# Optimization experiments

Measured on AMD Instinct MI355X. Metric: run time of the kernel, lower is better.

## Reference

```python
import jax, jax.numpy as jnp
import numpy as np

NUM_PAGES = 1024
PAGE_SIZE = 64
KV_HEADS = 8
HEAD_DIM = 128
NUM_TOKENS = 8192


def setup_inputs() -> dict:
    key = jax.random.key(0)
    k1, k2, k3 = jax.random.split(key, 3)
    kv_pages = jnp.zeros((NUM_PAGES, PAGE_SIZE, 2 * KV_HEADS, HEAD_DIM), dtype=jnp.float32)
    new_k = jax.random.normal(k1, (NUM_TOKENS, KV_HEADS, HEAD_DIM), dtype=jnp.float32)
    new_v = jax.random.normal(k2, (NUM_TOKENS, KV_HEADS, HEAD_DIM), dtype=jnp.float32)
    # distinct random destination slots (irregular but deterministic scatter);
    # mark a small tail as padding (-1) to exercise the drop path.
    dests = jax.random.permutation(k3, NUM_PAGES * PAGE_SIZE)[:NUM_TOKENS].astype(jnp.int32)
    pad = jnp.arange(NUM_TOKENS) >= (NUM_TOKENS - 128)
    token_dests = jnp.where(pad, jnp.int32(-1), dests)
    return {"kv_pages": kv_pages, "new_k": new_k, "new_v": new_v, "token_dests": token_dests}


def reference(kv_pages, new_k, new_v, token_dests):
    # kv_pages: [num_pages, page_size, 2*kv_heads, head_dim]
    # new_k/new_v: [tok, kv_heads, head_dim]; token_dests: i32[tok] flat slot index (-1 = pad)
    num_pages, page_size = kv_pages.shape[0], kv_pages.shape[1]
    kv_heads = new_k.shape[1]
    valid = token_dests >= 0
    t_pages = jnp.where(valid, token_dests // page_size, num_pages)   # OOB -> dropped
    t_slots = jnp.where(valid, token_dests % page_size, page_size)
    out = kv_pages.at[t_pages, t_slots, :kv_heads].set(new_k, mode="drop")
    out = out.at[t_pages, t_slots, kv_heads:].set(new_v, mode="drop")
    return out
```

## Files before the change

kernel.cpp:

```cpp
#include <hip/hip_runtime.h>


__global__ void kv_scatter_kernel(const float4* __restrict__ new_k,
                                  const float4* __restrict__ new_v,
                                  const int* __restrict__ dests,
                                  float4* __restrict__ out,
                                  int num_slots) {
    const int t = blockIdx.x;
    const int d = dests[t];
    if (d < 0 || d >= num_slots) return;

    const float4* __restrict__ k = new_k + (size_t)t * 256;
    const float4* __restrict__ v = new_v + (size_t)t * 256;
    float4* __restrict__ o = out + (size_t)d * 512;

    const int i = threadIdx.x;
    o[i]       = k[i];
    o[i + 256] = v[i];
}

extern "C" void kernel_launch(void* const* d_in, const int* in_sizes, int n_in,
                              void* d_out, int out_size, void* d_ws, size_t ws_size,
                              hipStream_t stream) {
    const float* kv_pages = (const float*)d_in[0];
    const float* new_k    = (const float*)d_in[1];
    const float* new_v    = (const float*)d_in[2];
    const int*   dests    = (const int*)d_in[3];

    const int num_tokens = in_sizes[3];
    const int row_floats = 2 * 8 * 128;
    const int num_slots  = out_size / row_floats;

    hipMemcpyAsync(d_out, kv_pages, (size_t)out_size * sizeof(float),
                   hipMemcpyDeviceToDevice, stream);

    kv_scatter_kernel<<<num_tokens, 256, 0, stream>>>(
        (const float4*)new_k, (const float4*)new_v, dests,
        (float4*)d_out, num_slots);
}
```

Before: 234.0 us.

## Fuse page copy and scatter via inverse slot map with nontemporal accesses

Builds an inverse map from destination slot to token in workspace, then a single grid-stride kernel writes every output row once, reading either the new K/V row or the original page row. This avoids copying the full cache and then overwriting the scattered slots, so the scattered rows are written once instead of twice. Loads and stores use nontemporal builtins to limit cache pollution. It adds two small kernel launches and depends on enough workspace being available, falling back to the old path otherwise.

```diff
diff --git a/kernel.cpp b/kernel.cpp
--- a/kernel.cpp
+++ b/kernel.cpp
@@ -1,19 +1,56 @@
 #include <hip/hip_runtime.h>
 
 
-__global__ void kv_scatter_kernel(const float4* __restrict__ new_k,
-                                  const float4* __restrict__ new_v,
+typedef float f4 __attribute__((ext_vector_type(4)));
+
+__global__ void inv_init_kernel(int* __restrict__ inv, int num_slots) {
+    const int stride = gridDim.x * blockDim.x;
+    for (int s = blockIdx.x * blockDim.x + threadIdx.x; s < num_slots; s += stride)
+        inv[s] = -1;
+}
+
+__global__ void inv_scatter_kernel(const int* __restrict__ dests, int num_tokens,
+                                   int* __restrict__ inv, int num_slots) {
+    const int t = blockIdx.x * blockDim.x + threadIdx.x;
+    if (t >= num_tokens) return;
+    const int d = dests[t];
+    if (d >= 0 && d < num_slots) inv[d] = t;
+}
+
+__global__ void fused_copy_scatter(const f4* __restrict__ kv_pages,
+                                   const f4* __restrict__ new_k,
+                                   const f4* __restrict__ new_v,
+                                   const int* __restrict__ inv,
+                                   f4* __restrict__ out,
+                                   int num_slots) {
+    const int i = threadIdx.x;
+    for (int slot = blockIdx.x; slot < num_slots; slot += gridDim.x) {
+        const int t = inv[slot];
+        f4* o = out + (size_t)slot * 512;
+        if (t >= 0) {
+            const f4* k = new_k + (size_t)t * 256;
+            const f4* v = new_v + (size_t)t * 256;
+            __builtin_nontemporal_store(__builtin_nontemporal_load(k + i), o + i);
+            __builtin_nontemporal_store(__builtin_nontemporal_load(v + i), o + i + 256);
+        } else {
+            const f4* src = kv_pages + (size_t)slot * 512;
+            __builtin_nontemporal_store(__builtin_nontemporal_load(src + i), o + i);
+            __builtin_nontemporal_store(__builtin_nontemporal_load(src + i + 256), o + i + 256);
+        }
+    }
+}
+
+__global__ void kv_scatter_kernel(const f4* __restrict__ new_k,
+                                  const f4* __restrict__ new_v,
                                   const int* __restrict__ dests,
-                                  float4* __restrict__ out,
+                                  f4* __restrict__ out,
                                   int num_slots) {
     const int t = blockIdx.x;
     const int d = dests[t];
     if (d < 0 || d >= num_slots) return;
-
-    const float4* __restrict__ k = new_k + (size_t)t * 256;
-    const float4* __restrict__ v = new_v + (size_t)t * 256;
-    float4* __restrict__ o = out + (size_t)d * 512;
-
+    const f4* k = new_k + (size_t)t * 256;
+    const f4* v = new_v + (size_t)t * 256;
+    f4* o = out + (size_t)d * 512;
     const int i = threadIdx.x;
     o[i]       = k[i];
     o[i + 256] = v[i];
@@ -31,10 +68,18 @@
     const int row_floats = 2 * 8 * 128;
     const int num_slots  = out_size / row_floats;
 
-    hipMemcpyAsync(d_out, kv_pages, (size_t)out_size * sizeof(float),
-                   hipMemcpyDeviceToDevice, stream);
-
-    kv_scatter_kernel<<<num_tokens, 256, 0, stream>>>(
-        (const float4*)new_k, (const float4*)new_v, dests,
-        (float4*)d_out, num_slots);
+    if (ws_size >= (size_t)num_slots * sizeof(int)) {
+        int* inv = (int*)d_ws;
+        inv_init_kernel<<<256, 256, 0, stream>>>(inv, num_slots);
+        inv_scatter_kernel<<<(num_tokens + 255) / 256, 256, 0, stream>>>(
+            dests, num_tokens, inv, num_slots);
+        fused_copy_scatter<<<2048, 256, 0, stream>>>(
+            (const f4*)kv_pages, (const f4*)new_k, (const f4*)new_v,
+            inv, (f4*)d_out, num_slots);
+    } else {
+        hipMemcpyAsync(d_out, kv_pages, (size_t)out_size * sizeof(float),
+                       hipMemcpyDeviceToDevice, stream);
+        kv_scatter_kernel<<<num_tokens, 256, 0, stream>>>(
+            (const f4*)new_k, (const f4*)new_v, dests, (f4*)d_out, num_slots);
+    }
 }
```

New measurement: 201.6 us. 1.16x faster.
